# Optimization experiments

Measured on AMD Instinct MI355X. Metric: run time of the kernel, lower is better.

Reference implementation:

```python
import jax, jax.numpy as jnp
import numpy as np
from jax import lax

DEPTH_SIZE = 16


def _conv2d(x, w, b):
    # x: [B,C,H,W], w: [O,I,5,5], 'SAME' == padding=2 for k=5
    y = lax.conv_general_dilated(x, w, (1, 1), 'SAME',
                                 dimension_numbers=('NCHW', 'OIHW', 'NCHW'))
    return y + b[None, :, None, None]


def _bn(x, g, b, m, v):
    # eval-mode BatchNorm2d, eps=1e-5
    scale = g / jnp.sqrt(v + 1e-5)
    return (x - m[None, :, None, None]) * scale[None, :, None, None] + b[None, :, None, None]


def setup_inputs() -> dict:
    key = jax.random.key(0)
    ks = jax.random.split(key, 24)
    f32 = jnp.float32
    B, H, W = 1, 384, 384

    def cw(k, shape):
        fan_in = float(np.prod(shape[1:]))
        return jax.random.normal(k, shape, f32) / np.float32(np.sqrt(fan_in))

    inp = {
        'light':     jax.random.uniform(ks[0], (B, 3, H, W), f32),
        'albedo':    jax.random.uniform(ks[1], (B, 3, H, W), f32),
        'normals':   jax.random.normal(ks[2], (B, 3, H, W), f32),
        'positions': jax.random.normal(ks[3], (B, 3, H, W), f32),
        'c1_w': cw(ks[4], (32, 9, 5, 5)),  'c1_b': jnp.zeros((32,), f32),
        'bn1_g': jax.random.uniform(ks[5], (32,), f32, 0.5, 1.5),
        'bn1_b': jax.random.normal(ks[6], (32,), f32) * 0.1,
        'bn1_m': jax.random.normal(ks[7], (32,), f32) * 0.1,
        'bn1_v': jax.random.uniform(ks[8], (32,), f32, 0.5, 1.5),
        'c2_w': cw(ks[9], (8, 32, 5, 5)),  'c2_b': jnp.zeros((8,), f32),
        'bn2_g': jax.random.uniform(ks[10], (8,), f32, 0.5, 1.5),
        'bn2_b': jax.random.normal(ks[11], (8,), f32) * 0.1,
        'bn2_m': jax.random.normal(ks[12], (8,), f32) * 0.1,
        'bn2_v': jax.random.uniform(ks[13], (8,), f32, 0.5, 1.5),
        'c3_w': cw(ks[14], (1, 8, 5, 5)),  'c3_b': jnp.zeros((1,), f32),
        'bn3_g': jax.random.uniform(ks[15], (1,), f32, 0.5, 1.5),
        'bn3_b': jax.random.normal(ks[16], (1,), f32) * 0.1,
        'bn3_m': jax.random.normal(ks[17], (1,), f32) * 0.1,
        'bn3_v': jax.random.uniform(ks[18], (1,), f32, 0.5, 1.5),
        'f_w': cw(ks[19], (4, 4, 7, 7, 7)),
        # weight-channel bias = 1 keeps the divide-by-weight well conditioned
        'f_b': jnp.concatenate([jnp.zeros((3,), f32), jnp.ones((1,), f32)]),
    }
    return inp


def reference(light, albedo, normals, positions,
              c1_w, c1_b, bn1_g, bn1_b, bn1_m, bn1_v,
              c2_w, c2_b, bn2_g, bn2_b, bn2_m, bn2_v,
              c3_w, c3_b, bn3_g, bn3_b, bn3_m, bn3_v,
              f_w, f_b):
    D = DEPTH_SIZE
    B, _, H, W = light.shape

    # estimate_depth CNN on cat(light, albedo, normals) -> sigmoid embedding in (0,1)
    x = jnp.concatenate([light, albedo, normals], axis=1)           # [B,9,H,W]
    h = jax.nn.relu(_bn(_conv2d(x, c1_w, c1_b), bn1_g, bn1_b, bn1_m, bn1_v))
    h = jax.nn.relu(_bn(_conv2d(h, c2_w, c2_b), bn2_g, bn2_b, bn2_m, bn2_v))
    emb = jax.nn.sigmoid(_bn(_conv2d(h, c3_w, c3_b), bn3_g, bn3_b, bn3_m, bn3_v))  # [B,1,H,W]

    # quantize depth into bin index (long() == floor for positive values)
    depth = jnp.floor(emb[:, 0] * (D - 1e-5)).astype(jnp.int32)     # [B,H,W], in [0,15]

    # project: scatter per-pixel (light, 1) into the 16-slot depth volume
    wl = jnp.concatenate([light, jnp.ones((B, 1, H, W), light.dtype)], axis=1)   # [B,4,H,W]
    onehot = (depth[:, None, :, :] == jnp.arange(D)[None, :, None, None]).astype(light.dtype)  # [B,D,H,W]
    vol = wl[:, :, None, :, :] * onehot[:, None, :, :, :]           # [B,4,D,H,W]

    # dense 7^3 Conv3d filter, padding=3 == 'SAME'
    fvol = lax.conv_general_dilated(vol, f_w, (1, 1, 1), 'SAME',
                                    dimension_numbers=('NCDHW', 'OIDHW', 'NCDHW'))
    fvol = fvol + f_b[None, :, None, None, None]                    # [B,4,D,H,W]

    # unproject: gather back at each pixel's depth bin
    idx = jnp.broadcast_to(depth[:, None, None, :, :], (B, 4, 1, H, W))
    gathered = jnp.take_along_axis(fvol, idx, axis=2)[:, :, 0]      # [B,4,H,W]

    filtered_light, weight = gathered[:, :3], gathered[:, 3:4]
    return (filtered_light / weight) * albedo                       # [B,3,H,W]
```

## Files before the change

kernel.cpp:

```cpp
#include <hip/hip_runtime.h>
#include <math.h>

#define HW 384
#define PLANE (HW*HW)

#define WT1_OFF   0
#define SC1_OFF   7296
#define SH1_OFF   7328
#define WT2_OFF   7360
#define SC2_OFF   13760
#define SH2_OFF   13768
#define W3_OFF    13776
#define SC3_OFF   13976
#define SH3_OFF   13977
#define FWT_OFF   13984
#define H1_OFF    32768
#define H2_OFF    (32768 + 32*PLANE)
#define DEPTH_OFF (32768 + 64*PLANE)

__global__ void prep_kernel(
    const float* __restrict__ c1w, const float* __restrict__ c1b,
    const float* __restrict__ g1, const float* __restrict__ b1,
    const float* __restrict__ m1, const float* __restrict__ v1,
    const float* __restrict__ c2w, const float* __restrict__ c2b,
    const float* __restrict__ g2, const float* __restrict__ b2,
    const float* __restrict__ m2, const float* __restrict__ v2,
    const float* __restrict__ c3w, const float* __restrict__ c3b,
    const float* __restrict__ g3, const float* __restrict__ b3,
    const float* __restrict__ m3, const float* __restrict__ v3,
    const float* __restrict__ fw, float* __restrict__ W)
{
    int gid = blockIdx.x * 256 + threadIdx.x;
    int gstr = gridDim.x * 256;
    for (int i = gid; i < 7200; i += gstr) {
        int gw = i / 450, r = i % 450;
        int c = r / 50, t = r % 50, tap = t >> 1, o = t & 1;
        int oc = (gw >> 2) * 8 + (gw & 3) * 2 + o;
        W[WT1_OFF + i] = c1w[oc * 225 + c * 25 + tap];
    }
    for (int i = gid; i < 6400; i += gstr) {
        int gw = i / 400, r = i % 400;
        int cc2 = r / 200, r2 = r % 200, tap = r2 >> 3, o = r2 & 7;
        int cab = (gw >> 2) * 8 + (gw & 3) * 2 + cc2;
        W[WT2_OFF + i] = c2w[o * 800 + cab * 25 + tap];
    }
    for (int i = gid; i < 6860; i += gstr) {
        int s = i / 20, k = i % 20;
        float v = 0.f;
        if (k < 16) { int o = k >> 2, c = k & 3; v = fw[o * 1372 + c * 343 + s]; }
        W[FWT_OFF + i] = v;
    }
    if (blockIdx.x == 0) {
        int tid = threadIdx.x;
        if (tid < 32) {
            float sc = g1[tid] / sqrtf(v1[tid] + 1e-5f);
            W[SC1_OFF + tid] = sc;
            W[SH1_OFF + tid] = (c1b[tid] - m1[tid]) * sc + b1[tid];
        }
        if (tid < 8) {
            float sc = g2[tid] / sqrtf(v2[tid] + 1e-5f);
            W[SC2_OFF + tid] = sc;
            W[SH2_OFF + tid] = (c2b[tid] - m2[tid]) * sc + b2[tid];
        }
        if (tid < 200) W[W3_OFF + tid] = c3w[tid];
        if (tid == 0) {
            float sc = g3[0] / sqrtf(v3[0] + 1e-5f);
            W[SC3_OFF] = sc;
            W[SH3_OFF] = (c3b[0] - m3[0]) * sc + b3[0];
        }
    }
}

__global__ __launch_bounds__(256, 4) void conv1_kernel(
    const float* __restrict__ light, const float* __restrict__ albedo,
    const float* __restrict__ normals, const float* __restrict__ W,
    float* __restrict__ h1)
{
    __shared__ __align__(16) float tile[9 * 432];
    int tid = threadIdx.x;
    int wu = __builtin_amdgcn_readfirstlane(tid >> 6);
    int slot = tid & 63;
    int qx = slot & 7, ty = slot >> 3;
    int bid = blockIdx.x;
    int g = bid & 3, sp = bid >> 2;
    int bx = sp % 12, by = sp / 12;
    int x0 = bx * 32, y0 = by * 8;

    for (int p = tid; p < 432; p += 256) {
        int py = p / 36, px = p % 36;
        int gy = y0 + py - 2, gx = x0 + px - 2;
        bool ok = ((unsigned)gy < (unsigned)HW) && ((unsigned)gx < (unsigned)HW);
        int gofs = ok ? (gy * HW + gx) : 0;
#pragma unroll
        for (int c = 0; c < 3; ++c) {
            float a = light[c * PLANE + gofs];
            float b = albedo[c * PLANE + gofs];
            float n = normals[c * PLANE + gofs];
            tile[(c    ) * 432 + p] = ok ? a : 0.f;
            tile[(c + 3) * 432 + p] = ok ? b : 0.f;
            tile[(c + 6) * 432 + p] = ok ? n : 0.f;
        }
    }
    __syncthreads();

    float acc[2][4];
#pragma unroll
    for (int o = 0; o < 2; ++o)
#pragma unroll
        for (int j = 0; j < 4; ++j) acc[o][j] = 0.f;

    int gw = g * 4 + wu;
    const float* wbase = W + WT1_OFF + gw * 450;
#pragma unroll 1
    for (int c = 0; c < 9; ++c) {
        const float* bc = tile + c * 432;
        const float* wc = wbase + c * 50;
#pragma unroll
        for (int ky = 0; ky < 5; ++ky) {
            const float* rp = bc + (ty + ky) * 36 + qx * 4;
            float4 ra = *(const float4*)rp;
            float4 rb = *(const float4*)(rp + 4);
            float row[8] = {ra.x, ra.y, ra.z, ra.w, rb.x, rb.y, rb.z, rb.w};
#pragma unroll
            for (int kx = 0; kx < 5; ++kx) {
                float2 wv = *(const float2*)(wc + (ky * 5 + kx) * 2);
#pragma unroll
                for (int j = 0; j < 4; ++j) {
                    float v = row[kx + j];
                    acc[0][j] = fmaf(v, wv.x, acc[0][j]);
                    acc[1][j] = fmaf(v, wv.y, acc[1][j]);
                }
            }
        }
    }

    int obase = g * 8 + 2 * wu;
    int pix = (y0 + ty) * HW + x0 + qx * 4;
#pragma unroll
    for (int o = 0; o < 2; ++o) {
        int oc = obase + o;
        float sc = W[SC1_OFF + oc], sh = W[SH1_OFF + oc];
        float4 rv;
        rv.x = fmaxf(fmaf(acc[o][0], sc, sh), 0.f);
        rv.y = fmaxf(fmaf(acc[o][1], sc, sh), 0.f);
        rv.z = fmaxf(fmaf(acc[o][2], sc, sh), 0.f);
        rv.w = fmaxf(fmaf(acc[o][3], sc, sh), 0.f);
        *(float4*)&h1[oc * PLANE + pix] = rv;
    }
}

__global__ __launch_bounds__(256, 4) void conv2_kernel(
    const float* __restrict__ h1, const float* __restrict__ W,
    float* __restrict__ h2p)
{
    __shared__ __align__(16) float lds[4608];
    int tid = threadIdx.x;
    int wu = __builtin_amdgcn_readfirstlane(tid >> 6);
    int slot = tid & 63;
    int qx = slot & 7, ty = slot >> 3;
    int bid = blockIdx.x;
    int q = bid & 3, sp = bid >> 2;
    int bx = sp % 12, by = sp / 12;
    int x0 = bx * 32, y0 = by * 8;
    int cbase = q * 8;

    for (int p = tid; p < 432; p += 256) {
        int py = p / 36, px = p % 36;
        int gy = y0 + py - 2, gx = x0 + px - 2;
        bool ok = ((unsigned)gy < (unsigned)HW) && ((unsigned)gx < (unsigned)HW);
        int gofs = ok ? (gy * HW + gx) : 0;
#pragma unroll
        for (int cc = 0; cc < 8; ++cc) {
            float v = h1[(cbase + cc) * PLANE + gofs];
            lds[cc * 432 + p] = ok ? v : 0.f;
        }
    }
    __syncthreads();

    float acc[8][4];
#pragma unroll
    for (int o = 0; o < 8; ++o)
#pragma unroll
        for (int j = 0; j < 4; ++j) acc[o][j] = 0.f;

    int gw = q * 4 + wu;
#pragma unroll 1
    for (int cc2 = 0; cc2 < 2; ++cc2) {
        const float* bc = lds + (2 * wu + cc2) * 432;
        const float* wc = W + WT2_OFF + gw * 400 + cc2 * 200;
#pragma unroll
        for (int ky = 0; ky < 5; ++ky) {
            const float* rp = bc + (ty + ky) * 36 + qx * 4;
            float4 ra = *(const float4*)rp;
            float4 rb = *(const float4*)(rp + 4);
            float row[8] = {ra.x, ra.y, ra.z, ra.w, rb.x, rb.y, rb.z, rb.w};
#pragma unroll
            for (int kx = 0; kx < 5; ++kx) {
                const float* wt = wc + (ky * 5 + kx) * 8;
                float4 wA = *(const float4*)wt;
                float4 wB = *(const float4*)(wt + 4);
#pragma unroll
                for (int j = 0; j < 4; ++j) {
                    float v = row[kx + j];
                    acc[0][j] = fmaf(v, wA.x, acc[0][j]);
                    acc[1][j] = fmaf(v, wA.y, acc[1][j]);
                    acc[2][j] = fmaf(v, wA.z, acc[2][j]);
                    acc[3][j] = fmaf(v, wA.w, acc[3][j]);
                    acc[4][j] = fmaf(v, wB.x, acc[4][j]);
                    acc[5][j] = fmaf(v, wB.y, acc[5][j]);
                    acc[6][j] = fmaf(v, wB.z, acc[6][j]);
                    acc[7][j] = fmaf(v, wB.w, acc[7][j]);
                }
            }
        }
    }
    __syncthreads();

    if (wu >= 2) {
        float* pp = lds + (wu - 2) * 2304 + slot * 36;
#pragma unroll
        for (int o = 0; o < 8; ++o)
            *(float4*)(pp + o * 4) = make_float4(acc[o][0], acc[o][1], acc[o][2], acc[o][3]);
    }
    __syncthreads();
    if (wu < 2) {
        const float* pp = lds + wu * 2304 + slot * 36;
#pragma unroll
        for (int o = 0; o < 8; ++o) {
            float4 t = *(const float4*)(pp + o * 4);
            acc[o][0] += t.x; acc[o][1] += t.y; acc[o][2] += t.z; acc[o][3] += t.w;
        }
    }
    __syncthreads();
    if (wu == 1) {
        float* pp = lds + slot * 36;
#pragma unroll
        for (int o = 0; o < 8; ++o)
            *(float4*)(pp + o * 4) = make_float4(acc[o][0], acc[o][1], acc[o][2], acc[o][3]);
    }
    __syncthreads();
    if (wu == 0) {
        const float* pp = lds + slot * 36;
        int pix = (y0 + ty) * HW + x0 + qx * 4;
#pragma unroll
        for (int o = 0; o < 8; ++o) {
            float4 t = *(const float4*)(pp + o * 4);
            float4 rv;
            rv.x = acc[o][0] + t.x; rv.y = acc[o][1] + t.y;
            rv.z = acc[o][2] + t.z; rv.w = acc[o][3] + t.w;
            *(float4*)&h2p[(q * 8 + o) * PLANE + pix] = rv;
        }
    }
}

__global__ __launch_bounds__(256, 2) void conv3_kernel(
    const float* __restrict__ h2p, const float* __restrict__ W,
    int* __restrict__ depth)
{
    __shared__ float tile[8 * 432];
    int tid = threadIdx.x;
    int tx = tid & 31, ty = tid >> 5;
    int bx = blockIdx.x % 12, by = blockIdx.x / 12;
    int x0 = bx * 32 - 2, y0 = by * 8 - 2;

    for (int p = tid; p < 432; p += 256) {
        int py = p / 36, px = p % 36;
        int gy = y0 + py, gx = x0 + px;
        bool ok = ((unsigned)gy < (unsigned)HW) && ((unsigned)gx < (unsigned)HW);
        int gofs = ok ? (gy * HW + gx) : 0;
#pragma unroll
        for (int c = 0; c < 8; ++c) {
            float t = ((h2p[c * PLANE + gofs] + h2p[(c + 8) * PLANE + gofs])
                     + h2p[(c + 16) * PLANE + gofs]) + h2p[(c + 24) * PLANE + gofs];
            float r = fmaxf(fmaf(t, W[SC2_OFF + c], W[SH2_OFF + c]), 0.f);
            tile[c * 432 + p] = ok ? r : 0.f;
        }
    }
    __syncthreads();

    float a = 0.f;
#pragma unroll 1
    for (int c = 0; c < 8; ++c) {
#pragma unroll
        for (int ky = 0; ky < 5; ++ky) {
#pragma unroll
            for (int kx = 0; kx < 5; ++kx) {
                a = fmaf(tile[c * 432 + (ty + ky) * 36 + tx + kx],
                         W[W3_OFF + (c * 5 + ky) * 5 + kx], a);
            }
        }
    }
    float y = fmaf(a, W[SC3_OFF], W[SH3_OFF]);
    float s = 1.f / (1.f + expf(-y));
    int d = (int)floorf(s * (16.f - 1e-5f));

    int gy = by * 8 + ty, gx = bx * 32 + tx;
    depth[gy * HW + gx] = d;
}

__global__ __launch_bounds__(256, 2) void final_kernel(
    const float* __restrict__ light, const float* __restrict__ albedo,
    const float* __restrict__ W, const float* __restrict__ fb,
    float* __restrict__ out)
{
    __shared__ __align__(16) float fwl[6860];
    __shared__ float ltile[3][14][38];
    __shared__ int   dtile[14][38];

    int tid = threadIdx.x;
    int tx = tid & 31, ty = tid >> 5;
    int bx = blockIdx.x % 12, by = blockIdx.x / 12;
    int x0 = bx * 32 - 3, y0 = by * 8 - 3;

    for (int i = tid; i < 6860; i += 256) fwl[i] = W[FWT_OFF + i];

    const int* dmap = ((const int*)W) + DEPTH_OFF;
    for (int p = tid; p < 14 * 38; p += 256) {
        int py = p / 38, px = p % 38;
        int gy = y0 + py, gx = x0 + px;
        bool ok = ((unsigned)gy < (unsigned)HW) && ((unsigned)gx < (unsigned)HW);
        int gofs = ok ? (gy * HW + gx) : 0;
        int dv = dmap[gofs];
        dtile[py][px] = ok ? dv : -1000;
#pragma unroll
        for (int c = 0; c < 3; ++c) {
            float lv = light[c * PLANE + gofs];
            ltile[c][py][px] = ok ? lv : 0.f;
        }
    }
    __syncthreads();

    int d0 = dtile[ty + 3][tx + 3];
    float a0 = fb[0], a1 = fb[1], a2 = fb[2], a3 = fb[3];

#pragma unroll 1
    for (int dy = 0; dy < 7; ++dy) {
#pragma unroll
        for (int dx = 0; dx < 7; ++dx) {
            int dd = dtile[ty + dy][tx + dx];
            int dz = dd - d0 + 3;
            if ((unsigned)dz < 7u) {
                int s = (dz * 7 + dy) * 7 + dx;
                const float* fs = fwl + s * 20;
                float4 w0 = *(const float4*)(fs);
                float4 w1 = *(const float4*)(fs + 4);
                float4 w2 = *(const float4*)(fs + 8);
                float4 w3 = *(const float4*)(fs + 12);
                float l0 = ltile[0][ty + dy][tx + dx];
                float l1 = ltile[1][ty + dy][tx + dx];
                float l2 = ltile[2][ty + dy][tx + dx];
                a0 += l0 * w0.x + l1 * w0.y + l2 * w0.z + w0.w;
                a1 += l0 * w1.x + l1 * w1.y + l2 * w1.z + w1.w;
                a2 += l0 * w2.x + l1 * w2.y + l2 * w2.z + w2.w;
                a3 += l0 * w3.x + l1 * w3.y + l2 * w3.z + w3.w;
            }
        }
    }

    int gy = by * 8 + ty, gx = bx * 32 + tx;
    int pix = gy * HW + gx;
    out[0 * PLANE + pix] = a0 / a3 * albedo[0 * PLANE + pix];
    out[1 * PLANE + pix] = a1 / a3 * albedo[1 * PLANE + pix];
    out[2 * PLANE + pix] = a2 / a3 * albedo[2 * PLANE + pix];
}

extern "C" void kernel_launch(void* const* d_in, const int* in_sizes, int n_in,
                              void* d_out, int out_size, void* d_ws, size_t ws_size,
                              hipStream_t stream) {
    const float* light     = (const float*)d_in[0];
    const float* albedo    = (const float*)d_in[1];
    const float* normals   = (const float*)d_in[2];
    const float* c1_w = (const float*)d_in[4];
    const float* c1_b = (const float*)d_in[5];
    const float* bn1_g = (const float*)d_in[6];
    const float* bn1_b = (const float*)d_in[7];
    const float* bn1_m = (const float*)d_in[8];
    const float* bn1_v = (const float*)d_in[9];
    const float* c2_w = (const float*)d_in[10];
    const float* c2_b = (const float*)d_in[11];
    const float* bn2_g = (const float*)d_in[12];
    const float* bn2_b = (const float*)d_in[13];
    const float* bn2_m = (const float*)d_in[14];
    const float* bn2_v = (const float*)d_in[15];
    const float* c3_w = (const float*)d_in[16];
    const float* c3_b = (const float*)d_in[17];
    const float* bn3_g = (const float*)d_in[18];
    const float* bn3_b = (const float*)d_in[19];
    const float* bn3_m = (const float*)d_in[20];
    const float* bn3_v = (const float*)d_in[21];
    const float* f_w = (const float*)d_in[22];
    const float* f_b = (const float*)d_in[23];

    float* W = (float*)d_ws;
    float* h1 = W + H1_OFF;
    float* h2p = W + H2_OFF;
    int* depth = ((int*)d_ws) + DEPTH_OFF;
    float* out = (float*)d_out;

    hipLaunchKernelGGL(prep_kernel, dim3(16), dim3(256), 0, stream,
                       c1_w, c1_b, bn1_g, bn1_b, bn1_m, bn1_v,
                       c2_w, c2_b, bn2_g, bn2_b, bn2_m, bn2_v,
                       c3_w, c3_b, bn3_g, bn3_b, bn3_m, bn3_v,
                       f_w, W);
    hipLaunchKernelGGL(conv1_kernel, dim3(2304), dim3(256), 0, stream,
                       light, albedo, normals, W, h1);
    hipLaunchKernelGGL(conv2_kernel, dim3(2304), dim3(256), 0, stream,
                       h1, W, h2p);
    hipLaunchKernelGGL(conv3_kernel, dim3(576), dim3(256), 0, stream,
                       h2p, W, depth);
    hipLaunchKernelGGL(final_kernel, dim3(576), dim3(256), 0, stream,
                       light, albedo, W, f_b, out);
}
```

Measured before the change: 99.96 us.

## Compute all 32 conv1 output channels per block with 8 channels per wave

Conv1 now has each block produce all 32 output channels for its spatial tile, with each wave accumulating 8 channels instead of 2. The weight layout in prep is reordered so each tap's 8 weights load as two float4 reads. This removes the fourfold redundant staging of the input tile in shared memory and reuses each loaded input row across more FMAs. In exchange the grid shrinks from 2304 to 576 blocks and each thread holds 32 accumulators, which lowers parallelism and raises register pressure.

New measurement: 95.93 us. 1.04x faster.

```diff
diff --git a/kernel.cpp b/kernel.cpp
--- a/kernel.cpp
+++ b/kernel.cpp
@@ -33,10 +33,10 @@
     int gid = blockIdx.x * 256 + threadIdx.x;
     int gstr = gridDim.x * 256;
     for (int i = gid; i < 7200; i += gstr) {
-        int gw = i / 450, r = i % 450;
-        int c = r / 50, t = r % 50, tap = t >> 1, o = t & 1;
-        int oc = (gw >> 2) * 8 + (gw & 3) * 2 + o;
-        W[WT1_OFF + i] = c1w[oc * 225 + c * 25 + tap];
+        int w = i / 1800, r = i % 1800;
+        int ct = r >> 3, o = r & 7;
+        int oc = w * 8 + o;
+        W[WT1_OFF + i] = c1w[oc * 225 + ct];
     }
     for (int i = gid; i < 6400; i += gstr) {
         int gw = i / 400, r = i % 400;
@@ -81,9 +81,7 @@
     int wu = __builtin_amdgcn_readfirstlane(tid >> 6);
     int slot = tid & 63;
     int qx = slot & 7, ty = slot >> 3;
-    int bid = blockIdx.x;
-    int g = bid & 3, sp = bid >> 2;
-    int bx = sp % 12, by = sp / 12;
+    int bx = blockIdx.x % 12, by = blockIdx.x / 12;
     int x0 = bx * 32, y0 = by * 8;
 
     for (int p = tid; p < 432; p += 256) {
@@ -103,18 +101,17 @@
     }
     __syncthreads();
 
-    float acc[2][4];
-#pragma unroll
-    for (int o = 0; o < 2; ++o)
+    float acc[8][4];
+#pragma unroll
+    for (int o = 0; o < 8; ++o)
 #pragma unroll
         for (int j = 0; j < 4; ++j) acc[o][j] = 0.f;
 
-    int gw = g * 4 + wu;
-    const float* wbase = W + WT1_OFF + gw * 450;
+    const float* wbase = W + WT1_OFF + wu * 1800;
 #pragma unroll 1
     for (int c = 0; c < 9; ++c) {
         const float* bc = tile + c * 432;
-        const float* wc = wbase + c * 50;
+        const float* wc = wbase + c * 200;
 #pragma unroll
         for (int ky = 0; ky < 5; ++ky) {
             const float* rp = bc + (ty + ky) * 36 + qx * 4;
@@ -123,22 +120,29 @@
             float row[8] = {ra.x, ra.y, ra.z, ra.w, rb.x, rb.y, rb.z, rb.w};
 #pragma unroll
             for (int kx = 0; kx < 5; ++kx) {
-                float2 wv = *(const float2*)(wc + (ky * 5 + kx) * 2);
+                const float* wt = wc + (ky * 5 + kx) * 8;
+                float4 wA = *(const float4*)wt;
+                float4 wB = *(const float4*)(wt + 4);
 #pragma unroll
                 for (int j = 0; j < 4; ++j) {
                     float v = row[kx + j];
-                    acc[0][j] = fmaf(v, wv.x, acc[0][j]);
-                    acc[1][j] = fmaf(v, wv.y, acc[1][j]);
+                    acc[0][j] = fmaf(v, wA.x, acc[0][j]);
+                    acc[1][j] = fmaf(v, wA.y, acc[1][j]);
+                    acc[2][j] = fmaf(v, wA.z, acc[2][j]);
+                    acc[3][j] = fmaf(v, wA.w, acc[3][j]);
+                    acc[4][j] = fmaf(v, wB.x, acc[4][j]);
+                    acc[5][j] = fmaf(v, wB.y, acc[5][j]);
+                    acc[6][j] = fmaf(v, wB.z, acc[6][j]);
+                    acc[7][j] = fmaf(v, wB.w, acc[7][j]);
                 }
             }
         }
     }
 
-    int obase = g * 8 + 2 * wu;
     int pix = (y0 + ty) * HW + x0 + qx * 4;
 #pragma unroll
-    for (int o = 0; o < 2; ++o) {
-        int oc = obase + o;
+    for (int o = 0; o < 8; ++o) {
+        int oc = wu * 8 + o;
         float sc = W[SC1_OFF + oc], sh = W[SH1_OFF + oc];
         float4 rv;
         rv.x = fmaxf(fmaf(acc[o][0], sc, sh), 0.f);
@@ -402,7 +406,7 @@
                        c2_w, c2_b, bn2_g, bn2_b, bn2_m, bn2_v,
                        c3_w, c3_b, bn3_g, bn3_b, bn3_m, bn3_v,
                        f_w, W);
-    hipLaunchKernelGGL(conv1_kernel, dim3(2304), dim3(256), 0, stream,
+    hipLaunchKernelGGL(conv1_kernel, dim3(576), dim3(256), 0, stream,
                        light, albedo, normals, W, h1);
     hipLaunchKernelGGL(conv2_kernel, dim3(2304), dim3(256), 0, stream,
                        h1, W, h2p);
```
